# Optimization experiments

Measured on AMD Instinct MI355X. Metric: run time of the kernel, lower is better.

Reference implementation:

```python
import jax, jax.numpy as jnp
import numpy as np
import math

TOPK = 13
NUM_CLASSES = 80
ALPHA = 1.0
BETA = 6.0
EPS = 1e-9


def setup_inputs() -> dict:
    key = jax.random.key(0)
    ks = jax.random.split(key, 7)
    bs, na, nc, ng = 16, 8400, 80, 128
    pd_scores = jax.random.uniform(ks[0], (bs, na, nc), dtype=jnp.float32)
    # valid xyxy predicted boxes: center in [0,640], w/h in [8,72]
    pc = jax.random.uniform(ks[1], (bs, na, 2), dtype=jnp.float32) * 640.0
    pwh = jax.random.uniform(ks[2], (bs, na, 2), dtype=jnp.float32) * 64.0 + 8.0
    pd_bboxes = jnp.concatenate([pc - pwh / 2, pc + pwh / 2], axis=-1)
    anc_points = jax.random.uniform(ks[3], (na, 2), dtype=jnp.float32) * 640.0
    gt_labels = jax.random.randint(ks[4], (bs, ng, 1), 0, nc, dtype=jnp.int64)
    gc = jax.random.uniform(ks[5], (bs, ng, 2), dtype=jnp.float32) * 640.0
    gwh = jax.random.uniform(ks[6], (bs, ng, 2), dtype=jnp.float32) * 128.0 + 16.0
    gt_bboxes = jnp.concatenate([gc - gwh / 2, gc + gwh / 2], axis=-1)
    gt_mask = jnp.ones((bs, ng, 1), dtype=jnp.float32)
    return {"pd_scores": pd_scores, "pd_bboxes": pd_bboxes, "anc_points": anc_points,
            "gt_labels": gt_labels, "gt_bboxes": gt_bboxes, "gt_mask": gt_mask}


def _ciou(b1, b2, eps=1e-7):
    # b1: (bs, na, 1, 4), b2: (bs, 1, ng, 4), xyxy format -> CIoU (bs, na, ng)
    b1x1, b1y1, b1x2, b1y2 = b1[..., 0], b1[..., 1], b1[..., 2], b1[..., 3]
    b2x1, b2y1, b2x2, b2y2 = b2[..., 0], b2[..., 1], b2[..., 2], b2[..., 3]
    inter = jnp.clip(jnp.minimum(b1x2, b2x2) - jnp.maximum(b1x1, b2x1), 0) * \
            jnp.clip(jnp.minimum(b1y2, b2y2) - jnp.maximum(b1y1, b2y1), 0)
    w1, h1 = b1x2 - b1x1, b1y2 - b1y1 + eps
    w2, h2 = b2x2 - b2x1, b2y2 - b2y1 + eps
    union = w1 * h1 + w2 * h2 - inter + eps
    iou = inter / union
    cw = jnp.maximum(b1x2, b2x2) - jnp.minimum(b1x1, b2x1)
    ch = jnp.maximum(b1y2, b2y2) - jnp.minimum(b1y1, b2y1)
    c2 = cw * cw + ch * ch + eps
    rho2 = ((b2x1 + b2x2 - b1x1 - b1x2) ** 2 + (b2y1 + b2y2 - b1y1 - b1y2) ** 2) / 4.0
    v = (4.0 / math.pi ** 2) * (jnp.arctan(w2 / h2) - jnp.arctan(w1 / h1)) ** 2
    alpha = jax.lax.stop_gradient(v / (v - iou + (1.0 + eps)))
    return iou - (rho2 / c2 + v * alpha)


def reference(pd_scores, pd_bboxes, anc_points, gt_labels, gt_bboxes, gt_mask):
    bs, na, nc = pd_scores.shape
    ng = gt_bboxes.shape[1]
    gt_m = gt_mask[..., 0]  # (bs, ng) float

    # --- anchors whose center lies inside each GT box: (bs, na, ng) ---
    lt = gt_bboxes[:, None, :, :2]                    # (bs, 1, ng, 2)
    rb = gt_bboxes[:, None, :, 2:]
    anc = anc_points[None, :, None, :]                # (1, na, 1, 2)
    deltas = jnp.concatenate([anc - lt, rb - anc], axis=-1)  # (bs, na, ng, 4)
    mask_in_gts = (deltas.min(axis=-1) > EPS)         # (bs, na, ng) bool
    mask_pos = mask_in_gts.astype(pd_scores.dtype) * gt_m[:, None, :]

    # --- alignment metric: score^alpha * CIoU^beta, masked ---
    iou = jnp.clip(_ciou(pd_bboxes[:, :, None, :], gt_bboxes[:, None, :, :]), 0.0)
    gl = gt_labels[..., 0].astype(jnp.int32)          # (bs, ng)
    idx = jnp.broadcast_to(gl[:, None, :], (bs, na, ng))
    target_scores_g = jnp.take_along_axis(pd_scores, idx, axis=2)  # (bs, na, ng)
    align = (target_scores_g ** ALPHA) * (iou ** BETA) * mask_pos

    # --- per-GT top-k anchors, scattered into (bs, na, ng) 0/1 mask ---
    mt = jnp.swapaxes(align, 1, 2)                    # (bs, ng, na)
    _, top_idx = jax.lax.top_k(mt, TOPK)              # (bs, ng, TOPK)
    bi = jnp.arange(bs)[:, None, None]
    gi = jnp.arange(ng)[None, :, None]
    is_in = jnp.zeros((bs, ng, na), jnp.int32).at[bi, gi, top_idx].set(1)
    is_in = jnp.swapaxes(is_in, 1, 2)                 # (bs, na, ng)
    is_in = is_in * (gt_m[:, None, :] > 0).astype(jnp.int32)
    is_in = jnp.where(align > 1e-9, is_in, 0)

    # --- conflict resolution (faithful to module's arithmetic) ---
    conflict = is_in.sum(axis=-1) > 1                 # (bs, na)
    best_gt = jnp.argmax(align, axis=-1)              # (bs, na)
    one_hot_best = jax.nn.one_hot(best_gt, ng, dtype=jnp.int32)
    keep = (~conflict)[..., None].astype(jnp.int32)
    resolved = is_in * keep + one_hot_best * keep
    is_in = jnp.where(conflict.any(), resolved, is_in)

    final_mask = is_in.sum(axis=-1) > 0               # (bs, na) bool
    target_gt_idx = jnp.argmax(is_in, axis=-1)        # (bs, na)

    # --- gather targets ---
    flat = jnp.arange(bs)[:, None] * ng + target_gt_idx
    target_cls = gl.reshape(-1)[flat]                 # (bs, na)
    target_bboxes = gt_bboxes.reshape(-1, 4)[flat]    # (bs, na, 4)
    target_scores = jax.nn.one_hot(target_cls, NUM_CLASSES, dtype=pd_scores.dtype)

    # --- normalized alignment ---
    is_in_f = is_in.astype(align.dtype)
    amf = align * is_in_f
    max_metrics = amf.max(axis=-1, keepdims=True)
    max_iou = (iou * is_in_f).max(axis=-1, keepdims=True)
    norm_align = (max_metrics * amf / (max_iou + 1e-9)).max(axis=-1, keepdims=True)
    target_scores = target_scores * norm_align
    return (target_cls, target_bboxes, target_scores, final_mask, norm_align)
```

## Files before the change

kernel.cpp:

```cpp
#include <hip/hip_runtime.h>
#include <math.h>

#pragma clang fp contract(off)

#define BS 16
#define NA 8400
#define NG 128
#define NC 80
#define KTOP 13
#define CAP 1024

#define OFF_COUNTS 0
#define OFF_BITS   (OFF_COUNTS + BS * NG * 4)
#define OFF_SELCNT (OFF_BITS + (size_t)BS * NA * 16)
#define OFF_FLAG   (OFF_SELCNT + (size_t)BS * NA * 4)
#define ZERO_END   (OFF_FLAG + 256)
#define OFF_PAIRS  ZERO_END
#define OFF_BESTV  (OFF_PAIRS + (size_t)BS * NG * CAP * 8)
#define OFF_BESTG  (OFF_BESTV + (size_t)BS * NA * 4)

#define OUT_CLS    0
#define OUT_BBOX   (BS * NA)
#define OUT_SCORES (OUT_BBOX + BS * NA * 4)
#define OUT_MASK   (OUT_SCORES + BS * NA * NC)
#define OUT_NORM   (OUT_MASK + BS * NA)

__device__ __forceinline__ float dev_ciou(float px1, float py1, float px2, float py2,
                                          float gx1, float gy1, float gx2, float gy2) {
    const float eps = 1e-7f;
    float iw = fminf(px2, gx2) - fmaxf(px1, gx1); iw = fmaxf(iw, 0.0f);
    float ih = fminf(py2, gy2) - fmaxf(py1, gy1); ih = fmaxf(ih, 0.0f);
    float inter = iw * ih;
    float w1 = px2 - px1;
    float h1 = (py2 - py1) + eps;
    float w2 = gx2 - gx1;
    float h2 = (gy2 - gy1) + eps;
    float uni = ((w1 * h1 + w2 * h2) - inter) + eps;
    float iou = inter / uni;
    float cw = fmaxf(px2, gx2) - fminf(px1, gx1);
    float ch = fmaxf(py2, gy2) - fminf(py1, gy1);
    float c2 = (cw * cw + ch * ch) + eps;
    float tx = ((gx1 + gx2) - px1) - px2;
    float ty = ((gy1 + gy2) - py1) - py2;
    float rho2 = (tx * tx + ty * ty) / 4.0f;
    float da = atanf(w2 / h2) - atanf(w1 / h1);
    float v = ((float)(4.0 / (M_PI * M_PI))) * (da * da);
    float alpha = v / ((v - iou) + (float)(1.0 + 1e-7));
    float res = iou - (rho2 / c2 + v * alpha);
    return fmaxf(res, 0.0f);
}

__global__ __launch_bounds__(256) void k_build(
    const float* __restrict__ scores, const float* __restrict__ pboxes,
    const float* __restrict__ anc, const int* __restrict__ glab,
    const float* __restrict__ gboxes, const float* __restrict__ gmask,
    unsigned int* __restrict__ counts, uint2* __restrict__ pairs,
    float* __restrict__ bestv, int* __restrict__ bestg)
{
    __shared__ float4 s_gb[NG];
    __shared__ int s_gl[NG];
    __shared__ float s_gm[NG];
    __shared__ unsigned long long s_best[64];
    __shared__ unsigned short s_q[64 * NG];
    __shared__ unsigned int s_qn;
    int b = blockIdx.y;
    int tid = threadIdx.x;
    if (tid == 0) s_qn = 0;
    for (int i = tid; i < NG; i += 256) {
        s_gb[i] = ((const float4*)gboxes)[b * NG + i];
        s_gl[i] = glab[b * NG + i];
        s_gm[i] = gmask[b * NG + i];
    }
    if (tid < 64) s_best[tid] = 127ULL;
    __syncthreads();

    int lane = tid & 63;
    int chunk = tid >> 6;
    int a0 = blockIdx.x * 64;
    int a = a0 + lane;
    bool valid = (a < NA);
    float ax = -1e30f, ay = -1e30f;
    if (valid) { ax = anc[a * 2 + 0]; ay = anc[a * 2 + 1]; }

    for (int j = 0; j < 32; j++) {
        int g = chunk * 32 + j;
        float4 gb = s_gb[g];
        float mn = fminf(fminf(ax - gb.x, ay - gb.y), fminf(gb.z - ax, gb.w - ay));
        if (valid && mn > 1e-9f && s_gm[g] != 0.0f) {
            unsigned int pos = atomicAdd(&s_qn, 1u);
            s_q[pos] = (unsigned short)((lane << 7) | g);
        }
    }
    __syncthreads();

    int qn = (int)s_qn;
    for (int i = tid; i < qn; i += 256) {
        int e = (int)s_q[i];
        int al_ = e >> 7, g = e & 127;
        int aa = a0 + al_;
        size_t t = (size_t)b * NA + aa;
        float4 gb = s_gb[g];
        float4 pb = ((const float4*)pboxes)[t];
        float iou = dev_ciou(pb.x, pb.y, pb.z, pb.w, gb.x, gb.y, gb.z, gb.w);
        float s = scores[t * NC + s_gl[g]];
        float al = (s * powf(iou, 6.0f)) * s_gm[g];
        if (al > 1e-9f) {
            int col = b * NG + g;
            unsigned int pos = atomicAdd(&counts[col], 1u);
            if (pos < CAP)
                pairs[(size_t)col * CAP + pos] = make_uint2(__float_as_uint(al), (unsigned int)aa);
        }
        unsigned long long key =
            ((unsigned long long)__float_as_uint(al) << 32) | (unsigned int)(127 - g);
        atomicMax(&s_best[al_], key);
    }
    __syncthreads();

    if (tid < 64 && a0 + tid < NA) {
        unsigned long long key = s_best[tid];
        size_t t = (size_t)b * NA + a0 + tid;
        bestv[t] = __uint_as_float((unsigned int)(key >> 32));
        bestg[t] = 127 - (int)(key & 0x7Fu);
    }
}

__global__ __launch_bounds__(256) void k_select(
    const unsigned int* __restrict__ counts, const uint2* __restrict__ pairs,
    const float* __restrict__ gmask,
    unsigned int* __restrict__ bits, unsigned int* __restrict__ selcnt,
    int* __restrict__ flag)
{
    __shared__ uint2 s_list[4][CAP];
    int wv = threadIdx.x >> 6, lane = threadIdx.x & 63;
    int col = blockIdx.x * 4 + wv;
    if (col >= BS * NG) return;
    if (!(gmask[col] > 0.0f)) return;
    int b = col >> 7, g = col & 127;
    int cnt = (int)counts[col]; if (cnt > CAP) cnt = CAP;
    uint2* lst = s_list[wv];
    for (int i = lane; i < cnt; i += 64) lst[i] = pairs[(size_t)col * CAP + i];
    int nch = (cnt + 63) >> 6;
    int nk = cnt < KTOP ? cnt : KTOP;
    for (int k = 0; k < nk; k++) {
        float bv = -1.0f; unsigned int ba = 0xFFFFFFFFu;
        for (int j = 0; j < nch; j++) {
            int i = lane + j * 64;
            if (i < cnt) {
                uint2 p = lst[i];
                float v = __uint_as_float(p.x);
                if (v > bv || (v == bv && p.y < ba)) { bv = v; ba = p.y; }
            }
        }
        for (int off = 1; off < 64; off <<= 1) {
            float ov = __shfl_xor(bv, off);
            unsigned int oa = (unsigned int)__shfl_xor((int)ba, off);
            if (ov > bv || (ov == bv && oa < ba)) { bv = ov; ba = oa; }
        }
        for (int j = 0; j < nch; j++) {
            int i = lane + j * 64;
            if (i < cnt && lst[i].y == ba) lst[i].x = __float_as_uint(-1.0f);
        }
        if (lane == 0) {
            size_t t = (size_t)b * NA + ba;
            atomicOr(&bits[t * 4 + (g >> 5)], 1u << (g & 31));
            unsigned int old = atomicAdd(&selcnt[t], 1u);
            if (old >= 1u) atomicOr(flag, 1);
        }
    }
}

__global__ __launch_bounds__(256) void k_final(
    const float* __restrict__ scores, const float* __restrict__ pboxes,
    const int* __restrict__ glab, const float* __restrict__ gboxes,
    const float* __restrict__ gmask,
    const unsigned int* __restrict__ bits, const int* __restrict__ flagp,
    const float* __restrict__ bestvp, const int* __restrict__ bestgp,
    float* __restrict__ o_cls, float* __restrict__ o_bbox, float* __restrict__ o_scores,
    float* __restrict__ o_mask, float* __restrict__ o_norm)
{
    __shared__ float4 s_gb[NG];
    __shared__ int s_gl[NG];
    __shared__ float s_gm[NG];
    int b = blockIdx.y;
    for (int i = threadIdx.x; i < NG; i += 256) {
        s_gb[i] = ((const float4*)gboxes)[b * NG + i];
        s_gl[i] = glab[b * NG + i];
        s_gm[i] = gmask[b * NG + i];
    }
    __syncthreads();
    int a = blockIdx.x * 256 + threadIdx.x;
    if (a >= NA) return;
    size_t t = (size_t)b * NA + a;
    unsigned int ew[4];
    ew[0] = bits[t * 4 + 0]; ew[1] = bits[t * 4 + 1];
    ew[2] = bits[t * 4 + 2]; ew[3] = bits[t * 4 + 3];
    int cnt = __popc(ew[0]) + __popc(ew[1]) + __popc(ew[2]) + __popc(ew[3]);
    bool conflict_any = (flagp[0] != 0);
    float best_v = bestvp[t]; int best_g = bestgp[t];
    float4 pb = ((const float4*)pboxes)[t];
    const float* srow = scores + t * NC;

    bool keep = (cnt <= 1);
    float M = 0.0f, mxiou = 0.0f;
    int tgt = 0;
    float fmask = 0.0f;

    if (!conflict_any) {
        fmask = (cnt > 0) ? 1.0f : 0.0f;
        for (int w = 0; w < 4; w++) {
            if (ew[w]) { tgt = w * 32 + __ffs(ew[w]) - 1; break; }
        }
        for (int w = 0; w < 4; w++) {
            unsigned int m = ew[w];
            while (m) {
                int j = __ffs(m) - 1; m &= m - 1;
                int g = w * 32 + j;
                float4 gb = s_gb[g];
                float iv = dev_ciou(pb.x, pb.y, pb.z, pb.w, gb.x, gb.y, gb.z, gb.w);
                float s = srow[s_gl[g]];
                float av = (s * powf(iv, 6.0f)) * s_gm[g];
                M = fmaxf(M, av);
                mxiou = fmaxf(mxiou, iv);
            }
        }
    } else if (!keep) {
        fmask = 0.0f; tgt = 0; M = 0.0f; mxiou = 0.0f;
    } else {
        fmask = 1.0f;
        bool eff_best = ((ew[best_g >> 5] >> (best_g & 31)) & 1u) != 0u;
        int first_eff = 1 << 30;
        for (int w = 0; w < 4; w++) {
            if (ew[w]) { first_eff = w * 32 + __ffs(ew[w]) - 1; break; }
        }
        tgt = eff_best ? best_g : (first_eff < best_g ? first_eff : best_g);
        for (int w = 0; w < 4; w++) {
            unsigned int m = ew[w];
            while (m) {
                int j = __ffs(m) - 1; m &= m - 1;
                int g = w * 32 + j;
                float r = (g == best_g) ? 2.0f : 1.0f;
                float4 gb = s_gb[g];
                float iv = dev_ciou(pb.x, pb.y, pb.z, pb.w, gb.x, gb.y, gb.z, gb.w);
                float s = srow[s_gl[g]];
                float av = (s * powf(iv, 6.0f)) * s_gm[g];
                M = fmaxf(M, av * r);
                mxiou = fmaxf(mxiou, iv * r);
            }
        }
        if (!eff_best) {
            float4 gb = s_gb[best_g];
            float iv = dev_ciou(pb.x, pb.y, pb.z, pb.w, gb.x, gb.y, gb.z, gb.w);
            M = fmaxf(M, best_v);
            mxiou = fmaxf(mxiou, iv);
        }
    }

    float norm = (M * M) / (mxiou + 1e-9f);
    int cls = s_gl[tgt];
    float4 gb = s_gb[tgt];
    o_cls[t] = (float)cls;
    ((float4*)o_bbox)[t] = gb;
    o_mask[t] = fmask;
    o_norm[t] = norm;
    float* orow = o_scores + t * (size_t)NC;
    #pragma unroll
    for (int j = 0; j < NC / 4; j++) {
        int base = j * 4;
        float4 z;
        z.x = (cls == base + 0) ? norm : 0.0f;
        z.y = (cls == base + 1) ? norm : 0.0f;
        z.z = (cls == base + 2) ? norm : 0.0f;
        z.w = (cls == base + 3) ? norm : 0.0f;
        ((float4*)orow)[j] = z;
    }
}

extern "C" void kernel_launch(void* const* d_in, const int* in_sizes, int n_in,
                              void* d_out, int out_size, void* d_ws, size_t ws_size,
                              hipStream_t stream) {
    const float* pd_scores = (const float*)d_in[0];
    const float* pd_bboxes = (const float*)d_in[1];
    const float* anc       = (const float*)d_in[2];
    const int*   glab      = (const int*)d_in[3];
    const float* gboxes    = (const float*)d_in[4];
    const float* gmask     = (const float*)d_in[5];
    float* out = (float*)d_out;

    char* ws = (char*)d_ws;
    unsigned int* counts = (unsigned int*)(ws + OFF_COUNTS);
    unsigned int* bits   = (unsigned int*)(ws + OFF_BITS);
    unsigned int* selcnt = (unsigned int*)(ws + OFF_SELCNT);
    int*          flag   = (int*)(ws + OFF_FLAG);
    uint2*        pairs  = (uint2*)(ws + OFF_PAIRS);
    float*        bestv  = (float*)(ws + OFF_BESTV);
    int*          bestg  = (int*)(ws + OFF_BESTG);

    hipMemsetAsync(ws, 0, ZERO_END, stream);

    k_build<<<dim3((NA + 63) / 64, BS), 256, 0, stream>>>(
        pd_scores, pd_bboxes, anc, glab, gboxes, gmask, counts, pairs, bestv, bestg);

    k_select<<<dim3(BS * NG / 4), 256, 0, stream>>>(
        counts, pairs, gmask, bits, selcnt, flag);

    k_final<<<dim3((NA + 255) / 256, BS), 256, 0, stream>>>(
        pd_scores, pd_bboxes, glab, gboxes, gmask, bits, flag, bestv, bestg,
        out + OUT_CLS, out + OUT_BBOX, out + OUT_SCORES, out + OUT_MASK, out + OUT_NORM);
}
```

Measured before the change: 139.4 us.

## Use ballot-based queues in build and register-resident top-k in select

```diff
diff --git a/kernel.cpp b/kernel.cpp
--- a/kernel.cpp
+++ b/kernel.cpp
@@ -16,8 +16,7 @@
 #define OFF_FLAG   (OFF_SELCNT + (size_t)BS * NA * 4)
 #define ZERO_END   (OFF_FLAG + 256)
 #define OFF_PAIRS  ZERO_END
-#define OFF_BESTV  (OFF_PAIRS + (size_t)BS * NG * CAP * 8)
-#define OFF_BESTG  (OFF_BESTV + (size_t)BS * NA * 4)
+#define OFF_BESTK  (OFF_PAIRS + (size_t)BS * NG * CAP * 8)
 
 #define OUT_CLS    0
 #define OUT_BBOX   (BS * NA)
@@ -55,17 +54,16 @@
     const float* __restrict__ anc, const int* __restrict__ glab,
     const float* __restrict__ gboxes, const float* __restrict__ gmask,
     unsigned int* __restrict__ counts, uint2* __restrict__ pairs,
-    float* __restrict__ bestv, int* __restrict__ bestg)
+    unsigned long long* __restrict__ bestkey)
 {
     __shared__ float4 s_gb[NG];
     __shared__ int s_gl[NG];
     __shared__ float s_gm[NG];
+    __shared__ unsigned short s_q[4][2048];
+    __shared__ int s_qlen[4];
     __shared__ unsigned long long s_best[64];
-    __shared__ unsigned short s_q[64 * NG];
-    __shared__ unsigned int s_qn;
     int b = blockIdx.y;
     int tid = threadIdx.x;
-    if (tid == 0) s_qn = 0;
     for (int i = tid; i < NG; i += 256) {
         s_gb[i] = ((const float4*)gboxes)[b * NG + i];
         s_gl[i] = glab[b * NG + i];
@@ -74,54 +72,57 @@
     if (tid < 64) s_best[tid] = 127ULL;
     __syncthreads();
 
-    int lane = tid & 63;
-    int chunk = tid >> 6;
+    int wv = tid >> 6, lane = tid & 63;
     int a0 = blockIdx.x * 64;
     int a = a0 + lane;
     bool valid = (a < NA);
     float ax = -1e30f, ay = -1e30f;
-    if (valid) { ax = anc[a * 2 + 0]; ay = anc[a * 2 + 1]; }
-
+    if (valid) { float2 ap = ((const float2*)anc)[a]; ax = ap.x; ay = ap.y; }
+    unsigned long long lmask = (1ULL << lane) - 1ULL;
+    unsigned short* q = s_q[wv];
+
+    int qn = 0;
     for (int j = 0; j < 32; j++) {
-        int g = chunk * 32 + j;
+        int g = wv * 32 + j;
         float4 gb = s_gb[g];
         float mn = fminf(fminf(ax - gb.x, ay - gb.y), fminf(gb.z - ax, gb.w - ay));
-        if (valid && mn > 1e-9f && s_gm[g] != 0.0f) {
-            unsigned int pos = atomicAdd(&s_qn, 1u);
-            s_q[pos] = (unsigned short)((lane << 7) | g);
-        }
-    }
+        bool hit = valid && (mn > 1e-9f) && (s_gm[g] != 0.0f);
+        unsigned long long bal = __ballot(hit);
+        if (hit) q[qn + __popcll(bal & lmask)] = (unsigned short)((lane << 7) | g);
+        qn += __popcll(bal);
+    }
+    if (lane == 0) s_qlen[wv] = qn;
     __syncthreads();
 
-    int qn = (int)s_qn;
-    for (int i = tid; i < qn; i += 256) {
-        int e = (int)s_q[i];
-        int al_ = e >> 7, g = e & 127;
-        int aa = a0 + al_;
-        size_t t = (size_t)b * NA + aa;
-        float4 gb = s_gb[g];
-        float4 pb = ((const float4*)pboxes)[t];
-        float iou = dev_ciou(pb.x, pb.y, pb.z, pb.w, gb.x, gb.y, gb.z, gb.w);
-        float s = scores[t * NC + s_gl[g]];
-        float al = (s * powf(iou, 6.0f)) * s_gm[g];
-        if (al > 1e-9f) {
-            int col = b * NG + g;
-            unsigned int pos = atomicAdd(&counts[col], 1u);
-            if (pos < CAP)
-                pairs[(size_t)col * CAP + pos] = make_uint2(__float_as_uint(al), (unsigned int)aa);
-        }
-        unsigned long long key =
-            ((unsigned long long)__float_as_uint(al) << 32) | (unsigned int)(127 - g);
-        atomicMax(&s_best[al_], key);
+    for (int s = 0; s < 4; s++) {
+        int len = s_qlen[s];
+        const unsigned short* qq = s_q[s];
+        for (int i = tid; i < len; i += 256) {
+            int e = (int)qq[i];
+            int al_ = e >> 7, g = e & 127;
+            int aa = a0 + al_;
+            size_t t = (size_t)b * NA + aa;
+            float4 gb = s_gb[g];
+            float4 pb = ((const float4*)pboxes)[t];
+            float iou = dev_ciou(pb.x, pb.y, pb.z, pb.w, gb.x, gb.y, gb.z, gb.w);
+            float sc = scores[t * NC + s_gl[g]];
+            float al = (sc * powf(iou, 6.0f)) * s_gm[g];
+            if (al > 1e-9f) {
+                int col = b * NG + g;
+                unsigned int pos = atomicAdd(&counts[col], 1u);
+                if (pos < CAP)
+                    pairs[(size_t)col * CAP + pos] =
+                        make_uint2(__float_as_uint(al), (unsigned int)aa);
+            }
+            unsigned long long key =
+                ((unsigned long long)__float_as_uint(al) << 32) | (unsigned int)(127 - g);
+            atomicMax(&s_best[al_], key);
+        }
     }
     __syncthreads();
 
-    if (tid < 64 && a0 + tid < NA) {
-        unsigned long long key = s_best[tid];
-        size_t t = (size_t)b * NA + a0 + tid;
-        bestv[t] = __uint_as_float((unsigned int)(key >> 32));
-        bestg[t] = 127 - (int)(key & 0x7Fu);
-    }
+    if (tid < 64 && a0 + tid < NA)
+        bestkey[(size_t)b * NA + a0 + tid] = s_best[tid];
 }
 
 __global__ __launch_bounds__(256) void k_select(
@@ -130,25 +131,29 @@
     unsigned int* __restrict__ bits, unsigned int* __restrict__ selcnt,
     int* __restrict__ flag)
 {
-    __shared__ uint2 s_list[4][CAP];
     int wv = threadIdx.x >> 6, lane = threadIdx.x & 63;
     int col = blockIdx.x * 4 + wv;
-    if (col >= BS * NG) return;
     if (!(gmask[col] > 0.0f)) return;
     int b = col >> 7, g = col & 127;
     int cnt = (int)counts[col]; if (cnt > CAP) cnt = CAP;
-    uint2* lst = s_list[wv];
-    for (int i = lane; i < cnt; i += 64) lst[i] = pairs[(size_t)col * CAP + i];
     int nch = (cnt + 63) >> 6;
-    int nk = cnt < KTOP ? cnt : KTOP;
-    for (int k = 0; k < nk; k++) {
+    float v[CAP / 64]; unsigned int ai[CAP / 64];
+    #pragma unroll
+    for (int j = 0; j < CAP / 64; j++) {
+        int i = j * 64 + lane;
+        if (i < cnt) {
+            uint2 p = pairs[(size_t)col * CAP + i];
+            v[j] = __uint_as_float(p.x); ai[j] = p.y;
+        } else { v[j] = -1.0f; ai[j] = 0xFFFFFFFFu; }
+    }
+    unsigned int wins[KTOP];
+    int nw = 0;
+    for (int k = 0; k < KTOP; k++) {
         float bv = -1.0f; unsigned int ba = 0xFFFFFFFFu;
-        for (int j = 0; j < nch; j++) {
-            int i = lane + j * 64;
-            if (i < cnt) {
-                uint2 p = lst[i];
-                float v = __uint_as_float(p.x);
-                if (v > bv || (v == bv && p.y < ba)) { bv = v; ba = p.y; }
+        #pragma unroll
+        for (int j = 0; j < CAP / 64; j++) {
+            if (j < nch) {
+                if (v[j] > bv || (v[j] == bv && ai[j] < ba)) { bv = v[j]; ba = ai[j]; }
             }
         }
         for (int off = 1; off < 64; off <<= 1) {
@@ -156,16 +161,29 @@
             unsigned int oa = (unsigned int)__shfl_xor((int)ba, off);
             if (ov > bv || (ov == bv && oa < ba)) { bv = ov; ba = oa; }
         }
-        for (int j = 0; j < nch; j++) {
-            int i = lane + j * 64;
-            if (i < cnt && lst[i].y == ba) lst[i].x = __float_as_uint(-1.0f);
-        }
-        if (lane == 0) {
-            size_t t = (size_t)b * NA + ba;
-            atomicOr(&bits[t * 4 + (g >> 5)], 1u << (g & 31));
-            unsigned int old = atomicAdd(&selcnt[t], 1u);
-            if (old >= 1u) atomicOr(flag, 1);
-        }
+        if (!(bv > 1e-9f)) break;
+        wins[k] = ba; nw = k + 1;
+        #pragma unroll
+        for (int j = 0; j < CAP / 64; j++) {
+            if (ai[j] == ba) v[j] = -1.0f;
+        }
+    }
+    if (lane == 0 && nw > 0) {
+        unsigned int olds[KTOP];
+        #pragma unroll
+        for (int k = 0; k < KTOP; k++) {
+            if (k < nw) {
+                size_t t = (size_t)b * NA + wins[k];
+                atomicOr(&bits[t * 4 + (g >> 5)], 1u << (g & 31));
+                olds[k] = atomicAdd(&selcnt[t], 1u);
+            }
+        }
+        bool c = false;
+        #pragma unroll
+        for (int k = 0; k < KTOP; k++) {
+            if (k < nw && olds[k] >= 1u) c = true;
+        }
+        if (c) atomicOr(flag, 1);
     }
 }
 
@@ -174,7 +192,7 @@
     const int* __restrict__ glab, const float* __restrict__ gboxes,
     const float* __restrict__ gmask,
     const unsigned int* __restrict__ bits, const int* __restrict__ flagp,
-    const float* __restrict__ bestvp, const int* __restrict__ bestgp,
+    const unsigned long long* __restrict__ bestkey,
     float* __restrict__ o_cls, float* __restrict__ o_bbox, float* __restrict__ o_scores,
     float* __restrict__ o_mask, float* __restrict__ o_norm)
 {
@@ -196,7 +214,9 @@
     ew[2] = bits[t * 4 + 2]; ew[3] = bits[t * 4 + 3];
     int cnt = __popc(ew[0]) + __popc(ew[1]) + __popc(ew[2]) + __popc(ew[3]);
     bool conflict_any = (flagp[0] != 0);
-    float best_v = bestvp[t]; int best_g = bestgp[t];
+    unsigned long long key = bestkey[t];
+    float best_v = __uint_as_float((unsigned int)(key >> 32));
+    int best_g = 127 - (int)(key & 0x7Fu);
     float4 pb = ((const float4*)pboxes)[t];
     const float* srow = scores + t * NC;
 
@@ -287,23 +307,22 @@
     float* out = (float*)d_out;
 
     char* ws = (char*)d_ws;
-    unsigned int* counts = (unsigned int*)(ws + OFF_COUNTS);
-    unsigned int* bits   = (unsigned int*)(ws + OFF_BITS);
-    unsigned int* selcnt = (unsigned int*)(ws + OFF_SELCNT);
-    int*          flag   = (int*)(ws + OFF_FLAG);
-    uint2*        pairs  = (uint2*)(ws + OFF_PAIRS);
-    float*        bestv  = (float*)(ws + OFF_BESTV);
-    int*          bestg  = (int*)(ws + OFF_BESTG);
+    unsigned int*       counts  = (unsigned int*)(ws + OFF_COUNTS);
+    unsigned int*       bits    = (unsigned int*)(ws + OFF_BITS);
+    unsigned int*       selcnt  = (unsigned int*)(ws + OFF_SELCNT);
+    int*                flag    = (int*)(ws + OFF_FLAG);
+    uint2*              pairs   = (uint2*)(ws + OFF_PAIRS);
+    unsigned long long* bestkey = (unsigned long long*)(ws + OFF_BESTK);
 
     hipMemsetAsync(ws, 0, ZERO_END, stream);
 
     k_build<<<dim3((NA + 63) / 64, BS), 256, 0, stream>>>(
-        pd_scores, pd_bboxes, anc, glab, gboxes, gmask, counts, pairs, bestv, bestg);
+        pd_scores, pd_bboxes, anc, glab, gboxes, gmask, counts, pairs, bestkey);
 
     k_select<<<dim3(BS * NG / 4), 256, 0, stream>>>(
         counts, pairs, gmask, bits, selcnt, flag);
 
     k_final<<<dim3((NA + 255) / 256, BS), 256, 0, stream>>>(
-        pd_scores, pd_bboxes, glab, gboxes, gmask, bits, flag, bestv, bestg,
+        pd_scores, pd_bboxes, glab, gboxes, gmask, bits, flag, bestkey,
         out + OUT_CLS, out + OUT_BBOX, out + OUT_SCORES, out + OUT_MASK, out + OUT_NORM);
 }
```

After: 142.8 us. +2.4%, slower.
